# Kernel tuning notes

Measured on AMD Instinct MI355X. Metric: run time of the kernel, lower is better.

Reference implementation:

```python
import jax, jax.numpy as jnp
from jax import lax
import numpy as np

D = 8        # domain_num
L = 12       # label_num
C = 9        # attr_num
W = 128      # window_size
B = 4096
EPS = 1e-5


def setup_inputs() -> dict:
    key = jax.random.key(0)
    ks = jax.random.split(key, 12)
    s = 0.05
    return {
        "x": jax.random.normal(ks[0], (B, C, 1, W), dtype=jnp.float32),
        "weights": jax.random.uniform(ks[1], (B, D), dtype=jnp.float32),
        # per-domain stacked parameters (leading dim D)
        "gamma": jnp.ones((D, C), dtype=jnp.float32),
        "beta": jnp.zeros((D, C), dtype=jnp.float32),
        "w1": jax.random.normal(ks[2], (D, 32, C, 9), dtype=jnp.float32) * s,
        "b1": jax.random.normal(ks[3], (D, 32), dtype=jnp.float32) * s,
        "w2": jax.random.normal(ks[4], (D, 64, 32, 9), dtype=jnp.float32) * s,
        "b2": jax.random.normal(ks[5], (D, 64), dtype=jnp.float32) * s,
        "fcw": jax.random.normal(ks[6], (D, L, 64 * 26), dtype=jnp.float32) * s,
        "fcb": jax.random.normal(ks[7], (D, L), dtype=jnp.float32) * s,
    }


def _maxpool2(h):
    # MaxPool along width, kernel 2 stride 2 (height is 1 and already squeezed)
    b, c, w = h.shape
    return h.reshape(b, c, w // 2, 2).max(axis=-1)


def _branch(x3, gamma, beta, w1, b1, w2, b2, fcw, fcb):
    # x3: [B, C, W]. BatchNorm2d in training mode: batch stats over (N, H, W).
    mean = x3.mean(axis=(0, 2), keepdims=True)
    var = x3.var(axis=(0, 2), keepdims=True)
    xn = (x3 - mean) * lax.rsqrt(var + EPS) * gamma[None, :, None] + beta[None, :, None]
    dn = ('NCH', 'OIH', 'NCH')
    h = lax.conv_general_dilated(xn, w1, (1,), 'VALID', dimension_numbers=dn)
    h = _maxpool2(jax.nn.relu(h + b1[None, :, None]))          # [B,32,60]
    h = lax.conv_general_dilated(h, w2, (1,), 'VALID', dimension_numbers=dn)
    h = _maxpool2(jax.nn.relu(h + b2[None, :, None]))          # [B,64,26]
    flat = h.reshape(h.shape[0], 64 * 26)
    return jax.nn.relu(flat @ fcw.T + fcb)                      # [B,L]


def reference(x, weights, gamma, beta, w1, b1, w2, b2, fcw, fcb):
    x3 = x[:, :, 0, :]  # squeeze height=1 -> [B,C,W]
    per_domain = jax.vmap(_branch, in_axes=(None, 0, 0, 0, 0, 0, 0, 0, 0))(
        x3, gamma, beta, w1, b1, w2, b2, fcw, fcb)              # [D,B,L]
    # vectorized form of the nested python-loop weighted sum over domains
    return jnp.einsum('bd,dbl->bl', weights, per_domain)        # [B,L]
```

## Files before the change

kernel.cpp:

```cpp
#include <hip/hip_runtime.h>
#include <hip/hip_bf16.h>

#define D 8
#define L 12
#define C 9
#define W 128
#define B 4096
#define EPS 1e-5f

typedef __attribute__((ext_vector_type(8))) short v8s;
typedef __attribute__((ext_vector_type(4))) float v4f;

#define OFF_STATS 0
#define OFF_B1E   18432
#define OFF_W1T   18688
#define OFF_W2T   39168
#define OFF_FCWP  112896

#define REGION 2336

__device__ inline unsigned short f2bf(float f) {
    unsigned u = __builtin_bit_cast(unsigned, f);
    u += 0x7FFFu + ((u >> 16) & 1u);
    return (unsigned short)(u >> 16);
}
__device__ inline unsigned pk2(float a, float b) {
    float2 f2; f2.x = a; f2.y = b;
    __hip_bfloat162 h = __float22bfloat162_rn(f2);
    unsigned u; __builtin_memcpy(&u, &h, 4);
    return u;
}

__global__ void stats_repack_kernel(const float* __restrict__ x,
                                    const float* __restrict__ w2,
                                    const float* __restrict__ fcw,
                                    float* __restrict__ ws,
                                    float* __restrict__ out) {
    const int t = threadIdx.x;
    __shared__ float red2[4][18];
    if (blockIdx.x < 1024) {
        const int rb = blockIdx.x * 4;
        const int w = t & 127, half = t >> 7;
        float s[9], s2[9];
        #pragma unroll
        for (int c = 0; c < 9; c++) { s[c] = 0.f; s2[c] = 0.f; }
        #pragma unroll
        for (int pass = 0; pass < 2; pass++) {
            const int row = rb + pass * 2 + half;
            const float* xr = x + (size_t)row * 1152 + w;
            #pragma unroll
            for (int c = 0; c < 9; c++) {
                float v = xr[c * 128];
                s[c] += v; s2[c] += v * v;
            }
        }
        #pragma unroll
        for (int c = 0; c < 9; c++) {
            #pragma unroll
            for (int off = 32; off >= 1; off >>= 1) {
                s[c]  += __shfl_down(s[c], off);
                s2[c] += __shfl_down(s2[c], off);
            }
        }
        if ((t & 63) == 0) {
            #pragma unroll
            for (int c = 0; c < 9; c++) {
                red2[t >> 6][c] = s[c]; red2[t >> 6][9 + c] = s2[c];
            }
        }
        __syncthreads();
        if (t < 18)
            ws[OFF_STATS + t * 1024 + blockIdx.x] =
                red2[0][t] + red2[1][t] + red2[2][t] + red2[3][t];
    } else if (blockIdx.x < 1152) {
        const int g = (blockIdx.x - 1024) * 4 + (t >> 6);
        const int lane = t & 63;
        const int d = g >> 6, o = g & 63;
        const float* src = w2 + (size_t)(d * 64 + o) * 288;
        short* dst = (short*)(ws + OFF_W2T) + (size_t)d * 18432 + o * 288;
        for (int i = lane; i < 288; i += 64) {
            int ic = i / 9, tap = i % 9;
            dst[tap * 32 + ic] = (short)f2bf(src[i]);
        }
    } else if (blockIdx.x < 1200) {
        const int g = (blockIdx.x - 1152) * 4 + (t >> 6);
        const int lane = t & 63;
        const int dl = g >> 1, half = g & 1;
        const float* src = fcw + (size_t)dl * 1664;
        short* dst = (short*)(ws + OFF_FCWP) + (size_t)dl * 1664;
        for (int i = half * 832 + lane; i < half * 832 + 832; i += 64) {
            int o = i / 26, p = i % 26;
            dst[p * 64 + o] = (short)f2bf(src[i]);
        }
    } else {
        const int base = (blockIdx.x - 1200) * 6144;
        float4 z; z.x = z.y = z.z = z.w = 0.f;
        float4* o4 = (float4*)(out + base);
        for (int i = t; i < 1536; i += 256) o4[i] = z;
    }
}

__global__ void fold1_kernel(const float* __restrict__ w1, const float* __restrict__ b1,
                             const float* __restrict__ gamma, const float* __restrict__ beta,
                             float* __restrict__ ws) {
    const int d = blockIdx.x, t = threadIdx.x;
    const int lane = t & 63, wv = t >> 6;
    __shared__ float g[9], bt[9];
    for (int c = wv; c < 9; c += 4) {
        float s = 0.f, s2 = 0.f;
        #pragma unroll
        for (int j = 0; j < 16; j++) {
            s  += ws[OFF_STATS + c * 1024 + lane + 64 * j];
            s2 += ws[OFF_STATS + (9 + c) * 1024 + lane + 64 * j];
        }
        #pragma unroll
        for (int off = 32; off >= 1; off >>= 1) {
            s  += __shfl_down(s, off);
            s2 += __shfl_down(s2, off);
        }
        if (lane == 0) {
            const float N = (float)B * (float)W;
            float m  = s / N;
            float vv = s2 / N - m * m;
            float inv = rsqrtf(vv + EPS);
            float gg = gamma[d * 9 + c] * inv;
            g[c] = gg; bt[c] = beta[d * 9 + c] - gg * m;
        }
    }
    __syncthreads();
    const int o = t >> 3, sub = t & 7;
    short* w1t = (short*)(ws + OFF_W1T);
    short* dst = w1t + (size_t)d * 5120 + o * 160;
    const float* src = w1 + ((size_t)(d * 32 + o)) * 81;
    float bias_part = 0.f;
    for (int tap = sub; tap < 10; tap += 8) {
        for (int c = 0; c < 16; c++) {
            float v = 0.f;
            if (tap < 9 && c < 9) {
                float wv2 = src[c * 9 + tap];
                v = wv2 * g[c];
                bias_part += wv2 * bt[c];
            }
            dst[tap * 16 + c] = (short)f2bf(v);
        }
    }
    bias_part += __shfl_xor(bias_part, 1);
    bias_part += __shfl_xor(bias_part, 2);
    bias_part += __shfl_xor(bias_part, 4);
    if (sub == 0) ws[OFF_B1E + d * 32 + o] = b1[d * 32 + o] + bias_part;
}

__global__ __launch_bounds__(256, 4)
void branch_kernel(const float* __restrict__ x,
                   const float* __restrict__ b2g,
                   const float* __restrict__ fcb,
                   const float* __restrict__ wts,
                   const float* __restrict__ ws,
                   float* __restrict__ out) {
    const int t = threadIdx.x;
    const int lane = t & 63;
    const int wv = t >> 6;
    const int d = blockIdx.y;
    const int b0 = blockIdx.x * 4;
    const short* w1t  = (const short*)(ws + OFF_W1T) + (size_t)d * 5120;
    const short* w2t  = (const short*)(ws + OFF_W2T) + (size_t)d * 18432;
    const short* fcwp = (const short*)(ws + OFF_FCWP) + (size_t)d * 12 * 1664;
    const float* b1e  = ws + OFF_B1E + d * 32;

    __shared__ __align__(16) short lds[4 * REGION];
    short* myr = &lds[wv * REGION];

    const int n = lane & 15, quad = lane >> 4;

    {
        const float* xrow = x + (size_t)(b0 + wv) * 1152;
        #pragma unroll
        for (int rep = 0; rep < 2; rep++) {
            const int w = lane + rep * 64;
            float v[9];
            #pragma unroll
            for (int c = 0; c < 9; c++) v[c] = xrow[c * 128 + w];
            uint4 lo, hi;
            lo.x = pk2(v[0], v[1]); lo.y = pk2(v[2], v[3]);
            lo.z = pk2(v[4], v[5]); lo.w = pk2(v[6], v[7]);
            hi.x = (unsigned)(unsigned short)f2bf(v[8]); hi.y = 0; hi.z = 0; hi.w = 0;
            *(uint4*)&myr[(0 * 144 + w) * 8] = lo;
            *(uint4*)&myr[(1 * 144 + w) * 8] = hi;
        }
        if (lane < 16) {
            uint4 z; z.x = z.y = z.z = z.w = 0;
            *(uint4*)&myr[(0 * 144 + 128 + lane) * 8] = z;
            *(uint4*)&myr[(1 * 144 + 128 + lane) * 8] = z;
        }
    }

    {
        const int qh = quad >> 1, ql = quad & 1;
        const float bias0 = b1e[n], bias1 = b1e[16 + n];
        v4f acc[8][2];
        #pragma unroll
        for (int mt = 0; mt < 8; mt++)
            #pragma unroll
            for (int nt = 0; nt < 2; nt++) { v4f z = {0.f,0.f,0.f,0.f}; acc[mt][nt] = z; }
        __builtin_amdgcn_s_setprio(1);
        #pragma unroll
        for (int s = 0; s < 5; s++) {
            v8s Bw0 = *(const v8s*)&w1t[n * 160 + (2 * s + qh) * 16 + ql * 8];
            v8s Bw1 = *(const v8s*)&w1t[(16 + n) * 160 + (2 * s + qh) * 16 + ql * 8];
            #pragma unroll
            for (int mt = 0; mt < 8; mt++) {
                const int row = mt * 16 + n + 2 * s + qh;
                v8s Af = *(const v8s*)&myr[(ql * 144 + row) * 8];
                acc[mt][0] = __builtin_amdgcn_mfma_f32_16x16x32_bf16(Af, Bw0, acc[mt][0], 0, 0, 0);
                acc[mt][1] = __builtin_amdgcn_mfma_f32_16x16x32_bf16(Af, Bw1, acc[mt][1], 0, 0, 0);
            }
        }
        __builtin_amdgcn_s_setprio(0);
        unsigned held[16];
        #pragma unroll
        for (int mt = 0; mt < 8; mt++)
            #pragma unroll
            for (int nt = 0; nt < 2; nt++) {
                const float bb = nt ? bias1 : bias0;
                float h0  = fmaxf(fmaxf(acc[mt][nt][0], acc[mt][nt][1]) + bb, 0.f);
                float h1v = fmaxf(fmaxf(acc[mt][nt][2], acc[mt][nt][3]) + bb, 0.f);
                held[mt * 2 + nt] = pk2(h0, h1v);
            }
        #pragma unroll
        for (int mt = 0; mt < 8; mt++) {
            const int p = mt * 8 + quad * 2;
            #pragma unroll
            for (int nt = 0; nt < 2; nt++) {
                const unsigned pr = held[mt * 2 + nt];
                const int plane = nt * 2 + (n >> 3);
                const int col = n & 7;
                if (p < 60)     myr[(plane * 73 + p) * 8 + col]     = (short)(pr & 0xFFFFu);
                if (p + 1 < 60) myr[(plane * 73 + p + 1) * 8 + col] = (short)(pr >> 16);
            }
        }
    }

    {
        float biasv[4];
        #pragma unroll
        for (int nt = 0; nt < 4; nt++) biasv[nt] = b2g[d * 64 + nt * 16 + n];
        v4f acc[4][4];
        #pragma unroll
        for (int mt = 0; mt < 4; mt++)
            #pragma unroll
            for (int nt = 0; nt < 4; nt++) { v4f z = {0.f,0.f,0.f,0.f}; acc[mt][nt] = z; }
        __builtin_amdgcn_s_setprio(1);
        for (int tap = 0; tap < 9; tap++) {
            v8s Bw[4];
            #pragma unroll
            for (int nt = 0; nt < 4; nt++)
                Bw[nt] = *(const v8s*)&w2t[(nt * 16 + n) * 288 + tap * 32 + quad * 8];
            #pragma unroll
            for (int mt = 0; mt < 4; mt++) {
                const int row = mt * 16 + n + tap;
                v8s Af = *(const v8s*)&myr[(quad * 73 + row) * 8];
                #pragma unroll
                for (int nt = 0; nt < 4; nt++)
                    acc[mt][nt] = __builtin_amdgcn_mfma_f32_16x16x32_bf16(Af, Bw[nt], acc[mt][nt], 0, 0, 0);
            }
        }
        __builtin_amdgcn_s_setprio(0);
        unsigned held[16];
        #pragma unroll
        for (int mt = 0; mt < 4; mt++)
            #pragma unroll
            for (int nt = 0; nt < 4; nt++) {
                float h0  = fmaxf(fmaxf(acc[mt][nt][0], acc[mt][nt][1]) + biasv[nt], 0.f);
                float h1v = fmaxf(fmaxf(acc[mt][nt][2], acc[mt][nt][3]) + biasv[nt], 0.f);
                held[mt * 4 + nt] = pk2(h0, h1v);
            }
        #pragma unroll
        for (int mt = 0; mt < 4; mt++) {
            const int p = mt * 8 + quad * 2;
            #pragma unroll
            for (int nt = 0; nt < 4; nt++) {
                const unsigned pr = held[mt * 4 + nt];
                const int oc = nt * 16 + n;
                if (p < 26) {
                    const int gs = (oc >> 3) ^ (p & 7);
                    myr[p * 64 + gs * 8 + (oc & 7)] = (short)(pr & 0xFFFFu);
                }
                if (p + 1 < 26) {
                    const int gs = (oc >> 3) ^ ((p + 1) & 7);
                    myr[(p + 1) * 64 + gs * 8 + (oc & 7)] = (short)(pr >> 16);
                }
            }
        }
    }
    __syncthreads();

    {
        const int lrow = (n < 12) ? n : 0;
        v4f acc = {0.f, 0.f, 0.f, 0.f};
        __builtin_amdgcn_s_setprio(1);
        for (int ks = wv; ks < 52; ks += 4) {
            const int p = ks >> 1;
            const int gs = ((ks & 1) * 4 + quad) ^ (p & 7);
            v8s A  = *(const v8s*)&fcwp[lrow * 1664 + ks * 32 + quad * 8];
            v8s Bf = *(const v8s*)&lds[(n & 3) * REGION + p * 64 + gs * 8];
            acc = __builtin_amdgcn_mfma_f32_16x16x32_bf16(A, Bf, acc, 0, 0, 0);
        }
        __builtin_amdgcn_s_setprio(0);
        float* red = (float*)(myr + 1672);
        *(float4*)&red[lane * 4] = *(float4*)&acc;
    }
    __syncthreads();
    if (t < 64) {
        float sum[4] = {0.f, 0.f, 0.f, 0.f};
        #pragma unroll
        for (int w = 0; w < 4; w++) {
            const float* redw = (const float*)(&lds[w * REGION + 1672]);
            float4 v = *(const float4*)&redw[lane * 4];
            sum[0] += v.x; sum[1] += v.y; sum[2] += v.z; sum[3] += v.w;
        }
        if (n < 4) {
            const float wgt = wts[(size_t)(b0 + n) * 8 + d];
            #pragma unroll
            for (int r = 0; r < 4; r++) {
                const int l = quad * 4 + r;
                if (l < 12) {
                    float v = fmaxf(sum[r] + fcb[d * 12 + l], 0.f);
                    atomicAdd(&out[(size_t)(b0 + n) * 12 + l], wgt * v);
                }
            }
        }
    }
}

extern "C" void kernel_launch(void* const* d_in, const int* in_sizes, int n_in,
                              void* d_out, int out_size, void* d_ws, size_t ws_size,
                              hipStream_t stream) {
    const float* x       = (const float*)d_in[0];
    const float* weights = (const float*)d_in[1];
    const float* gamma   = (const float*)d_in[2];
    const float* beta    = (const float*)d_in[3];
    const float* w1      = (const float*)d_in[4];
    const float* b1      = (const float*)d_in[5];
    const float* w2      = (const float*)d_in[6];
    const float* b2      = (const float*)d_in[7];
    const float* fcw     = (const float*)d_in[8];
    const float* fcb     = (const float*)d_in[9];
    float* ws  = (float*)d_ws;
    float* out = (float*)d_out;

    stats_repack_kernel<<<dim3(1208), 256, 0, stream>>>(x, w2, fcw, ws, out);
    fold1_kernel<<<dim3(D), 256, 0, stream>>>(w1, b1, gamma, beta, ws);
    branch_kernel<<<dim3(B / 4, D), 256, 0, stream>>>(x, b2, fcb, weights, ws, out);
}
```

Baseline: 236.6 us.

## Switch conv stages to 32x32x16 MFMA tiles with per-tap K layout

Both convolution stages move from 16x16x32 bf16 MFMA to 32x32x16 bf16 MFMA. Conv1 now runs per tap with a K of 16 (9 channels padded) instead of packing tap pairs into K=32. Conv2 splits each tap's 32 input channels into two K=16 steps. The larger tiles reduce the number of B-fragment loads and MFMA issues per output, but conv1 now spends more padded K (9 taps × 16 versus 5 × 32), and the epilogue writes single bf16 values instead of packed pairs. The s_setprio hints are also removed.

```diff
diff --git a/kernel.cpp b/kernel.cpp
--- a/kernel.cpp
+++ b/kernel.cpp
@@ -10,6 +10,7 @@
 
 typedef __attribute__((ext_vector_type(8))) short v8s;
 typedef __attribute__((ext_vector_type(4))) float v4f;
+typedef __attribute__((ext_vector_type(16))) float v16f;
 
 #define OFF_STATS 0
 #define OFF_B1E   18432
@@ -171,6 +172,7 @@
     short* myr = &lds[wv * REGION];
 
     const int n = lane & 15, quad = lane >> 4;
+    const int m31 = lane & 31, hi = lane >> 5;
 
     {
         const float* xrow = x + (size_t)(b0 + wv) * 1152;
@@ -180,12 +182,12 @@
             float v[9];
             #pragma unroll
             for (int c = 0; c < 9; c++) v[c] = xrow[c * 128 + w];
-            uint4 lo, hi;
+            uint4 lo, hivec;
             lo.x = pk2(v[0], v[1]); lo.y = pk2(v[2], v[3]);
             lo.z = pk2(v[4], v[5]); lo.w = pk2(v[6], v[7]);
-            hi.x = (unsigned)(unsigned short)f2bf(v[8]); hi.y = 0; hi.z = 0; hi.w = 0;
+            hivec.x = (unsigned)(unsigned short)f2bf(v[8]); hivec.y = 0; hivec.z = 0; hivec.w = 0;
             *(uint4*)&myr[(0 * 144 + w) * 8] = lo;
-            *(uint4*)&myr[(1 * 144 + w) * 8] = hi;
+            *(uint4*)&myr[(1 * 144 + w) * 8] = hivec;
         }
         if (lane < 16) {
             uint4 z; z.x = z.y = z.z = z.w = 0;
@@ -195,99 +197,66 @@
     }
 
     {
-        const int qh = quad >> 1, ql = quad & 1;
-        const float bias0 = b1e[n], bias1 = b1e[16 + n];
-        v4f acc[8][2];
-        #pragma unroll
-        for (int mt = 0; mt < 8; mt++)
-            #pragma unroll
-            for (int nt = 0; nt < 2; nt++) { v4f z = {0.f,0.f,0.f,0.f}; acc[mt][nt] = z; }
-        __builtin_amdgcn_s_setprio(1);
-        #pragma unroll
-        for (int s = 0; s < 5; s++) {
-            v8s Bw0 = *(const v8s*)&w1t[n * 160 + (2 * s + qh) * 16 + ql * 8];
-            v8s Bw1 = *(const v8s*)&w1t[(16 + n) * 160 + (2 * s + qh) * 16 + ql * 8];
-            #pragma unroll
-            for (int mt = 0; mt < 8; mt++) {
-                const int row = mt * 16 + n + 2 * s + qh;
-                v8s Af = *(const v8s*)&myr[(ql * 144 + row) * 8];
-                acc[mt][0] = __builtin_amdgcn_mfma_f32_16x16x32_bf16(Af, Bw0, acc[mt][0], 0, 0, 0);
-                acc[mt][1] = __builtin_amdgcn_mfma_f32_16x16x32_bf16(Af, Bw1, acc[mt][1], 0, 0, 0);
-            }
-        }
-        __builtin_amdgcn_s_setprio(0);
-        unsigned held[16];
-        #pragma unroll
-        for (int mt = 0; mt < 8; mt++)
-            #pragma unroll
-            for (int nt = 0; nt < 2; nt++) {
-                const float bb = nt ? bias1 : bias0;
-                float h0  = fmaxf(fmaxf(acc[mt][nt][0], acc[mt][nt][1]) + bb, 0.f);
-                float h1v = fmaxf(fmaxf(acc[mt][nt][2], acc[mt][nt][3]) + bb, 0.f);
-                held[mt * 2 + nt] = pk2(h0, h1v);
-            }
-        #pragma unroll
-        for (int mt = 0; mt < 8; mt++) {
-            const int p = mt * 8 + quad * 2;
-            #pragma unroll
-            for (int nt = 0; nt < 2; nt++) {
-                const unsigned pr = held[mt * 2 + nt];
-                const int plane = nt * 2 + (n >> 3);
-                const int col = n & 7;
-                if (p < 60)     myr[(plane * 73 + p) * 8 + col]     = (short)(pr & 0xFFFFu);
-                if (p + 1 < 60) myr[(plane * 73 + p + 1) * 8 + col] = (short)(pr >> 16);
+        const float bias = b1e[m31];
+        v16f acc[4];
+        #pragma unroll
+        for (int mt = 0; mt < 4; mt++) acc[mt] = (v16f)(0.f);
+        for (int tap = 0; tap < 9; tap++) {
+            v8s Bw = *(const v8s*)&w1t[m31 * 160 + tap * 16 + hi * 8];
+            #pragma unroll
+            for (int mt = 0; mt < 4; mt++) {
+                v8s Af = *(const v8s*)&myr[(hi * 144 + mt * 32 + m31 + tap) * 8];
+                acc[mt] = __builtin_amdgcn_mfma_f32_32x32x16_bf16(Af, Bw, acc[mt], 0, 0, 0);
+            }
+        }
+        const int plane = m31 >> 3, col = m31 & 7;
+        #pragma unroll
+        for (int mt = 0; mt < 4; mt++) {
+            #pragma unroll
+            for (int j = 0; j < 8; j++) {
+                const int p = mt * 16 + 4 * (j >> 1) + (j & 1) + 2 * hi;
+                if (p < 60) {
+                    float h = fmaxf(fmaxf(acc[mt][2 * j], acc[mt][2 * j + 1]) + bias, 0.f);
+                    myr[(plane * 73 + p) * 8 + col] = (short)f2bf(h);
+                }
             }
         }
     }
 
     {
-        float biasv[4];
-        #pragma unroll
-        for (int nt = 0; nt < 4; nt++) biasv[nt] = b2g[d * 64 + nt * 16 + n];
-        v4f acc[4][4];
-        #pragma unroll
-        for (int mt = 0; mt < 4; mt++)
-            #pragma unroll
-            for (int nt = 0; nt < 4; nt++) { v4f z = {0.f,0.f,0.f,0.f}; acc[mt][nt] = z; }
-        __builtin_amdgcn_s_setprio(1);
-        for (int tap = 0; tap < 9; tap++) {
-            v8s Bw[4];
-            #pragma unroll
-            for (int nt = 0; nt < 4; nt++)
-                Bw[nt] = *(const v8s*)&w2t[(nt * 16 + n) * 288 + tap * 32 + quad * 8];
-            #pragma unroll
-            for (int mt = 0; mt < 4; mt++) {
-                const int row = mt * 16 + n + tap;
-                v8s Af = *(const v8s*)&myr[(quad * 73 + row) * 8];
-                #pragma unroll
-                for (int nt = 0; nt < 4; nt++)
-                    acc[mt][nt] = __builtin_amdgcn_mfma_f32_16x16x32_bf16(Af, Bw[nt], acc[mt][nt], 0, 0, 0);
-            }
-        }
-        __builtin_amdgcn_s_setprio(0);
-        unsigned held[16];
-        #pragma unroll
-        for (int mt = 0; mt < 4; mt++)
-            #pragma unroll
-            for (int nt = 0; nt < 4; nt++) {
-                float h0  = fmaxf(fmaxf(acc[mt][nt][0], acc[mt][nt][1]) + biasv[nt], 0.f);
-                float h1v = fmaxf(fmaxf(acc[mt][nt][2], acc[mt][nt][3]) + biasv[nt], 0.f);
-                held[mt * 4 + nt] = pk2(h0, h1v);
-            }
-        #pragma unroll
-        for (int mt = 0; mt < 4; mt++) {
-            const int p = mt * 8 + quad * 2;
-            #pragma unroll
-            for (int nt = 0; nt < 4; nt++) {
-                const unsigned pr = held[mt * 4 + nt];
-                const int oc = nt * 16 + n;
+        const float bias0 = b2g[d * 64 + m31];
+        const float bias1 = b2g[d * 64 + 32 + m31];
+        v16f acc[2][2];
+        #pragma unroll
+        for (int mt = 0; mt < 2; mt++)
+            #pragma unroll
+            for (int nt = 0; nt < 2; nt++) acc[mt][nt] = (v16f)(0.f);
+        for (int s = 0; s < 18; s++) {
+            const int tap = s >> 1, koff = (s & 1) * 16 + hi * 8;
+            v8s Bw0 = *(const v8s*)&w2t[m31 * 288 + tap * 32 + koff];
+            v8s Bw1 = *(const v8s*)&w2t[(32 + m31) * 288 + tap * 32 + koff];
+            const int aplane = (s & 1) * 2 + hi;
+            #pragma unroll
+            for (int mt = 0; mt < 2; mt++) {
+                v8s Af = *(const v8s*)&myr[(aplane * 73 + mt * 32 + m31 + tap) * 8];
+                acc[mt][0] = __builtin_amdgcn_mfma_f32_32x32x16_bf16(Af, Bw0, acc[mt][0], 0, 0, 0);
+                acc[mt][1] = __builtin_amdgcn_mfma_f32_32x32x16_bf16(Af, Bw1, acc[mt][1], 0, 0, 0);
+            }
+        }
+        #pragma unroll
+        for (int mt = 0; mt < 2; mt++) {
+            #pragma unroll
+            for (int j = 0; j < 8; j++) {
+                const int p = mt * 16 + 4 * (j >> 1) + (j & 1) + 2 * hi;
                 if (p < 26) {
-                    const int gs = (oc >> 3) ^ (p & 7);
-                    myr[p * 64 + gs * 8 + (oc & 7)] = (short)(pr & 0xFFFFu);
-                }
-                if (p + 1 < 26) {
-                    const int gs = (oc >> 3) ^ ((p + 1) & 7);
-                    myr[(p + 1) * 64 + gs * 8 + (oc & 7)] = (short)(pr >> 16);
+                    #pragma unroll
+                    for (int nt = 0; nt < 2; nt++) {
+                        const int oc = nt * 32 + m31;
+                        float h = fmaxf(fmaxf(acc[mt][nt][2 * j], acc[mt][nt][2 * j + 1])
+                                        + (nt ? bias1 : bias0), 0.f);
+                        const int gs = (oc >> 3) ^ (p & 7);
+                        myr[p * 64 + gs * 8 + (oc & 7)] = (short)f2bf(h);
+                    }
                 }
             }
         }
@@ -297,7 +266,6 @@
     {
         const int lrow = (n < 12) ? n : 0;
         v4f acc = {0.f, 0.f, 0.f, 0.f};
-        __builtin_amdgcn_s_setprio(1);
         for (int ks = wv; ks < 52; ks += 4) {
             const int p = ks >> 1;
             const int gs = ((ks & 1) * 4 + quad) ^ (p & 7);
@@ -305,7 +273,6 @@
             v8s Bf = *(const v8s*)&lds[(n & 3) * REGION + p * 64 + gs * 8];
             acc = __builtin_amdgcn_mfma_f32_16x16x32_bf16(A, Bf, acc, 0, 0, 0);
         }
-        __builtin_amdgcn_s_setprio(0);
         float* red = (float*)(myr + 1672);
         *(float4*)&red[lane * 4] = *(float4*)&acc;
     }
```

New measurement: 238.9 us. Within noise of the previous version (+1.0%).

## Repack conv1 im2col K dimension to cut MFMA steps from five to three

Applied to the files above, without the earlier changes.

Conv1 weights are repacked so the reduction dimension is 96 instead of 160. Eight channels across eight taps fill two K-chunks, and a third chunk gathers channel 8 and tap 8 from a second diagonal LDS strip built from channel 8 values. This cuts the conv1 MFMA count from 10 per output tile to 6 and drops the padded zero work. The s_setprio calls around all MFMA loops are also removed. The cost is more complex LDS staging with scattered 2-byte stores and address logic that depends on lane.

```diff
diff --git a/kernel.cpp b/kernel.cpp
--- a/kernel.cpp
+++ b/kernel.cpp
@@ -18,6 +18,7 @@
 #define OFF_FCWP  112896
 
 #define REGION 2336
+#define STRIP  1152
 
 __device__ inline unsigned short f2bf(float f) {
     unsigned u = __builtin_bit_cast(unsigned, f);
@@ -104,9 +105,9 @@
                              const float* __restrict__ gamma, const float* __restrict__ beta,
                              float* __restrict__ ws) {
     const int d = blockIdx.x, t = threadIdx.x;
-    const int lane = t & 63, wv = t >> 6;
+    const int lane = t & 63, wvq = t >> 6;
     __shared__ float g[9], bt[9];
-    for (int c = wv; c < 9; c += 4) {
+    for (int c = wvq; c < 9; c += 4) {
         float s = 0.f, s2 = 0.f;
         #pragma unroll
         for (int j = 0; j < 16; j++) {
@@ -130,19 +131,25 @@
     __syncthreads();
     const int o = t >> 3, sub = t & 7;
     short* w1t = (short*)(ws + OFF_W1T);
-    short* dst = w1t + (size_t)d * 5120 + o * 160;
+    short* dst = w1t + (size_t)d * 3072 + o * 96;
     const float* src = w1 + ((size_t)(d * 32 + o)) * 81;
+    for (int k = sub * 12; k < sub * 12 + 12; k++) {
+        int tap, ch;
+        if (k < 64)      { tap = (k >> 5) * 4 + ((k >> 3) & 3); ch = k & 7; }
+        else {
+            int q = (k >> 3) & 3, j = k & 7;
+            if (q == 0)              { tap = 8; ch = j; }
+            else if (q == 2)         { tap = j; ch = 8; }
+            else if (q == 3 && j==0) { tap = 8; ch = 8; }
+            else                     { tap = -1; ch = 0; }
+        }
+        float v = (tap >= 0) ? src[ch * 9 + tap] * g[ch] : 0.f;
+        dst[k] = (short)f2bf(v);
+    }
     float bias_part = 0.f;
-    for (int tap = sub; tap < 10; tap += 8) {
-        for (int c = 0; c < 16; c++) {
-            float v = 0.f;
-            if (tap < 9 && c < 9) {
-                float wv2 = src[c * 9 + tap];
-                v = wv2 * g[c];
-                bias_part += wv2 * bt[c];
-            }
-            dst[tap * 16 + c] = (short)f2bf(v);
-        }
+    for (int tap = sub; tap < 9; tap += 8) {
+        for (int c = 0; c < 9; c++)
+            bias_part += src[c * 9 + tap] * bt[c];
     }
     bias_part += __shfl_xor(bias_part, 1);
     bias_part += __shfl_xor(bias_part, 2);
@@ -162,7 +169,7 @@
     const int wv = t >> 6;
     const int d = blockIdx.y;
     const int b0 = blockIdx.x * 4;
-    const short* w1t  = (const short*)(ws + OFF_W1T) + (size_t)d * 5120;
+    const short* w1t  = (const short*)(ws + OFF_W1T) + (size_t)d * 3072;
     const short* w2t  = (const short*)(ws + OFF_W2T) + (size_t)d * 18432;
     const short* fcwp = (const short*)(ws + OFF_FCWP) + (size_t)d * 12 * 1664;
     const float* b1e  = ws + OFF_B1E + d * 32;
@@ -174,48 +181,59 @@
 
     {
         const float* xrow = x + (size_t)(b0 + wv) * 1152;
+        unsigned short c8s[2];
         #pragma unroll
         for (int rep = 0; rep < 2; rep++) {
             const int w = lane + rep * 64;
             float v[9];
             #pragma unroll
             for (int c = 0; c < 9; c++) v[c] = xrow[c * 128 + w];
-            uint4 lo, hi;
+            uint4 lo;
             lo.x = pk2(v[0], v[1]); lo.y = pk2(v[2], v[3]);
             lo.z = pk2(v[4], v[5]); lo.w = pk2(v[6], v[7]);
-            hi.x = (unsigned)(unsigned short)f2bf(v[8]); hi.y = 0; hi.z = 0; hi.w = 0;
-            *(uint4*)&myr[(0 * 144 + w) * 8] = lo;
-            *(uint4*)&myr[(1 * 144 + w) * 8] = hi;
-        }
-        if (lane < 16) {
+            *(uint4*)&myr[w * 8] = lo;
+            c8s[rep] = f2bf(v[8]);
+        }
+        {
             uint4 z; z.x = z.y = z.z = z.w = 0;
-            *(uint4*)&myr[(0 * 144 + 128 + lane) * 8] = z;
-            *(uint4*)&myr[(1 * 144 + 128 + lane) * 8] = z;
+            if (lane < 16) *(uint4*)&myr[(128 + lane) * 8] = z;
+            if (lane < 24) *(uint4*)&myr[STRIP + (120 + lane) * 8] = z;
+        }
+        #pragma unroll
+        for (int rep = 0; rep < 2; rep++) {
+            const int w = lane + rep * 64;
+            const short c8 = (short)c8s[rep];
+            #pragma unroll
+            for (int j = 0; j < 8; j++) {
+                if (rep == 1 || lane >= j)
+                    myr[STRIP + (w - j) * 8 + j] = c8;
+            }
         }
     }
 
     {
-        const int qh = quad >> 1, ql = quad & 1;
         const float bias0 = b1e[n], bias1 = b1e[16 + n];
         v4f acc[8][2];
         #pragma unroll
         for (int mt = 0; mt < 8; mt++)
             #pragma unroll
             for (int nt = 0; nt < 2; nt++) { v4f z = {0.f,0.f,0.f,0.f}; acc[mt][nt] = z; }
-        __builtin_amdgcn_s_setprio(1);
-        #pragma unroll
-        for (int s = 0; s < 5; s++) {
-            v8s Bw0 = *(const v8s*)&w1t[n * 160 + (2 * s + qh) * 16 + ql * 8];
-            v8s Bw1 = *(const v8s*)&w1t[(16 + n) * 160 + (2 * s + qh) * 16 + ql * 8];
+        #pragma unroll
+        for (int ck = 0; ck < 3; ck++) {
+            v8s Bw0 = *(const v8s*)&w1t[n * 96 + ck * 32 + quad * 8];
+            v8s Bw1 = *(const v8s*)&w1t[(16 + n) * 96 + ck * 32 + quad * 8];
             #pragma unroll
             for (int mt = 0; mt < 8; mt++) {
-                const int row = mt * 16 + n + 2 * s + qh;
-                v8s Af = *(const v8s*)&myr[(ql * 144 + row) * 8];
+                const int rowm = mt * 16 + n;
+                int aoff;
+                if (ck < 2) aoff = (rowm + ck * 4 + quad) * 8;
+                else        aoff = (quad < 2) ? (rowm + 8) * 8
+                                              : (STRIP + (rowm + (quad - 2) * 8) * 8);
+                v8s Af = *(const v8s*)&myr[aoff];
                 acc[mt][0] = __builtin_amdgcn_mfma_f32_16x16x32_bf16(Af, Bw0, acc[mt][0], 0, 0, 0);
                 acc[mt][1] = __builtin_amdgcn_mfma_f32_16x16x32_bf16(Af, Bw1, acc[mt][1], 0, 0, 0);
             }
         }
-        __builtin_amdgcn_s_setprio(0);
         unsigned held[16];
         #pragma unroll
         for (int mt = 0; mt < 8; mt++)
@@ -249,7 +267,6 @@
         for (int mt = 0; mt < 4; mt++)
             #pragma unroll
             for (int nt = 0; nt < 4; nt++) { v4f z = {0.f,0.f,0.f,0.f}; acc[mt][nt] = z; }
-        __builtin_amdgcn_s_setprio(1);
         for (int tap = 0; tap < 9; tap++) {
             v8s Bw[4];
             #pragma unroll
@@ -264,7 +281,6 @@
                     acc[mt][nt] = __builtin_amdgcn_mfma_f32_16x16x32_bf16(Af, Bw[nt], acc[mt][nt], 0, 0, 0);
             }
         }
-        __builtin_amdgcn_s_setprio(0);
         unsigned held[16];
         #pragma unroll
         for (int mt = 0; mt < 4; mt++)
@@ -297,7 +313,6 @@
     {
         const int lrow = (n < 12) ? n : 0;
         v4f acc = {0.f, 0.f, 0.f, 0.f};
-        __builtin_amdgcn_s_setprio(1);
         for (int ks = wv; ks < 52; ks += 4) {
             const int p = ks >> 1;
             const int gs = ((ks & 1) * 4 + quad) ^ (p & 7);
@@ -305,7 +320,6 @@
             v8s Bf = *(const v8s*)&lds[(n & 3) * REGION + p * 64 + gs * 8];
             acc = __builtin_amdgcn_mfma_f32_16x16x32_bf16(A, Bf, acc, 0, 0, 0);
         }
-        __builtin_amdgcn_s_setprio(0);
         float* red = (float*)(myr + 1672);
         *(float4*)&red[lane * 4] = *(float4*)&acc;
     }
```

After: 223.0 us. 5.7% less time.
